# Performance work log

Hardware: AMD Instinct MI355X
Metric: run time of the kernel (lower is better)

## Reference

```python
import jax, jax.numpy as jnp
import numpy as np

B, C, W, H, N = 8, 128, 48, 48, 8192


def setup_inputs() -> dict:
    key = jax.random.key(0)
    ks = jax.random.split(key, 16)
    s = 1.0 / np.sqrt(C)
    inp = {
        "feat0": jax.random.normal(ks[0], (B, C, W, H), jnp.float32),
        "feat1": jax.random.normal(ks[1], (B, C, N), jnp.float32),
        "geo_embed": jax.random.normal(ks[2], (B, W * H, C), jnp.float32),
        # Linear weights stored as [in, out]; biases [out].
        "Wq": jax.random.normal(ks[3], (C, C), jnp.float32) * s,
        "bq": jnp.zeros((C,), jnp.float32),
        "Wk": jax.random.normal(ks[4], (C, C), jnp.float32) * s,
        "bk": jnp.zeros((C,), jnp.float32),
        "Wv": jax.random.normal(ks[5], (C, C), jnp.float32) * s,
        "bv": jnp.zeros((C,), jnp.float32),
        "Wo": jax.random.normal(ks[6], (C, C), jnp.float32) * s,
        "bo": jnp.zeros((C,), jnp.float32),
        "Wg": jax.random.normal(ks[7], (C, C), jnp.float32) * s,
        "bg": jnp.zeros((C,), jnp.float32),
        "Wgate": jax.random.normal(ks[8], (2 * C, 1), jnp.float32) * (1.0 / np.sqrt(2 * C)),
        "bgate": jnp.zeros((1,), jnp.float32),
    }
    return inp


def reference(feat0, feat1, geo_embed, Wq, bq, Wk, bk, Wv, bv, Wo, bo, Wg, bg, Wgate, bgate):
    b, c, w, h = feat0.shape
    # b c w h -> b (w h) c
    q_in = feat0.reshape(b, c, w * h).transpose(0, 2, 1)
    pq = q_in @ Wq + bq  # [b, wh, c]

    geo = geo_embed @ Wg + bg  # [b, wh, c]
    gate = jax.nn.sigmoid(jnp.concatenate([pq, geo], axis=-1) @ Wgate + bgate)  # [b, wh, 1]
    pq = pq + gate * geo

    kv_in = feat1.transpose(0, 2, 1)  # [b, n, c]
    pk = kv_in @ Wk + bk
    pv = kv_in @ Wv + bv

    energy = jnp.einsum('bqc,bnc->bqn', pq, pk)  # [b, wh, n]
    # NOTE: original scales AFTER softmax (non-standard, faithful):
    attention = jax.nn.softmax(energy, axis=-1) / jnp.sqrt(jnp.asarray(c, energy.dtype))
    out = jnp.einsum('bqn,bnc->bqc', attention, pv) @ Wo + bo  # [b, wh, c]
    out = out.transpose(0, 2, 1).reshape(b, c, w, h)

    geo_r = geo.transpose(0, 2, 1).reshape(b, c, w, h)
    out = out * (1.0 + jax.nn.sigmoid(geo_r))
    out = out + feat0
    return out
```

## Files before the change

kernel.cpp:

```cpp
#include <hip/hip_runtime.h>

#define B_ 8
#define C_ 128
#define WH_ 2304
#define N_ 8192

typedef unsigned short u16;
typedef float f32x4 __attribute__((ext_vector_type(4)));
typedef short s16x8 __attribute__((ext_vector_type(8)));
typedef short s16x4 __attribute__((ext_vector_type(4)));
typedef unsigned int u32x2 __attribute__((ext_vector_type(2)));

typedef const unsigned int __attribute__((address_space(1))) ga_u32;
typedef unsigned int __attribute__((address_space(3))) lds_u32;

#define LOG2E 1.4426950408889634f
#define MOFF  64.0f

__device__ __forceinline__ float bf2f(u16 u){
    union { unsigned int i; float f; } x; x.i = ((unsigned int)u) << 16; return x.f;
}
__device__ __forceinline__ u16 f2bf(float f){
    union { float f; unsigned int i; } x; x.f = f;
    unsigned int r = x.i + 0x7fffu + ((x.i >> 16) & 1u);
    return (u16)(r >> 16);
}
__device__ __forceinline__ unsigned int cvtpk(float a, float b){
    unsigned int r;
    asm("v_cvt_pk_bf16_f32 %0, %1, %2" : "=v"(r) : "v"(a), "v"(b));
    return r;
}
__device__ __forceinline__ int swz(int row, int col){
    return row*128 + ((((col >> 3) ^ (row & 15)) << 3) | (col & 7));
}
__device__ __forceinline__ f32x4 fzero(){ f32x4 z = {0.f, 0.f, 0.f, 0.f}; return z; }
__device__ __forceinline__ f32x4 fmoff(){ f32x4 z = {-MOFF, -MOFF, -MOFF, -MOFF}; return z; }
__device__ __forceinline__ f32x4 mfma16(s16x8 a, s16x8 b, f32x4 c){
    return __builtin_amdgcn_mfma_f32_16x16x32_bf16(a, b, c, 0, 0, 0);
}
__device__ __forceinline__ void gld16(const void* g, void* l){
    __builtin_amdgcn_global_load_lds((ga_u32*)g, (lds_u32*)l, 16, 0, 0);
}
__device__ __forceinline__ s16x8 ldsf(const u16* p){ return *(const s16x8*)p; }
__device__ __forceinline__ s16x8 cvt8(const float* p){
    s16x8 r;
    #pragma unroll
    for (int j = 0; j < 8; j++) r[j] = (short)f2bf(p[j]);
    return r;
}

__global__ __launch_bounds__(256) void k_prep(
    const float* __restrict__ Wq, const float* __restrict__ Wk,
    const float* __restrict__ Wv, const float* __restrict__ Wo,
    const float* __restrict__ Wg, u16* __restrict__ Wt)
{
    const int gid = blockIdx.x*256 + threadIdx.x;
    const int mi = gid >> 14, e = gid & 16383;
    const int o = e >> 7, i = e & 127;
    const float* src = (mi==0)?Wq:(mi==1)?Wk:(mi==2)?Wv:(mi==3)?Wo:Wg;
    Wt[mi*16384 + o*128 + i] = f2bf(src[i*128 + o]);
}

__device__ __forceinline__ void proj_kv_body(
    u16* SB, int blk,
    const float* __restrict__ feat1,
    const float* __restrict__ bk, const float* __restrict__ bv,
    const u16* __restrict__ Wt,
    u16* __restrict__ Kb, u16* __restrict__ Vb)
{
    const int t = threadIdx.x;
    const int b = blk >> 7;
    const int n0 = (blk & 127) * 64;
    const int lane = t & 63, w = t >> 6, qq = lane >> 4, m = lane & 15;
    const int nr = n0 + w*16 + m;
    s16x8 aA[4];
    #pragma unroll
    for (int kt = 0; kt < 4; kt++){
        #pragma unroll
        for (int j = 0; j < 8; j++)
            aA[kt][j] = (short)f2bf(feat1[((size_t)b*C_ + kt*32 + qq*8 + j)*N_ + nr]);
    }
    const u16* WkT = Wt + 16384;
    const u16* WvT = Wt + 32768;
    f32x4 acc[8];
    #pragma unroll
    for (int ct = 0; ct < 8; ct++) acc[ct] = fzero();
    #pragma unroll
    for (int kt = 0; kt < 4; kt++){
        #pragma unroll
        for (int ct = 0; ct < 8; ct++){
            const s16x8 bf = *(const s16x8*)&WkT[(ct*16 + m)*128 + kt*32 + qq*8];
            acc[ct] = mfma16(aA[kt], bf, acc[ct]);
        }
    }
    #pragma unroll
    for (int ct = 0; ct < 8; ct++){
        const int col = ct*16 + m;
        const float bkv = bk[col];
        #pragma unroll
        for (int i = 0; i < 4; i++)
            SB[swz(w*16 + qq*4 + i, col)] = f2bf(acc[ct][i] + bkv);
    }
    #pragma unroll
    for (int j = 0; j < 4; j++){
        const int chunk = j*64 + lane;
        const int row = w*16 + (chunk >> 4);
        const int cb = chunk & 15;
        s16x8 v = ldsf(&SB[row*128 + ((cb ^ (row & 15)) << 3)]);
        *(s16x8*)&Kb[((size_t)b*N_ + n0 + row)*C_ + cb*8] = v;
    }
    #pragma unroll
    for (int ct = 0; ct < 8; ct++) acc[ct] = fzero();
    #pragma unroll
    for (int kt = 0; kt < 4; kt++){
        #pragma unroll
        for (int ct = 0; ct < 8; ct++){
            const s16x8 bf = *(const s16x8*)&WvT[(ct*16 + m)*128 + kt*32 + qq*8];
            acc[ct] = mfma16(aA[kt], bf, acc[ct]);
        }
    }
    #pragma unroll
    for (int ct = 0; ct < 8; ct++){
        const int col = ct*16 + m;
        const float bvv = bv[col];
        u32x2 pk;
        pk.x = cvtpk(acc[ct][0] + bvv, acc[ct][1] + bvv);
        pk.y = cvtpk(acc[ct][2] + bvv, acc[ct][3] + bvv);
        *(u32x2*)&Vb[((size_t)b*C_ + col)*N_ + n0 + w*16 + qq*4] = pk;
    }
}

__device__ __forceinline__ void proj_qg_body(
    u16* SB, int blk,
    const float* __restrict__ feat0, const float* __restrict__ geo,
    const float* __restrict__ bq, const float* __restrict__ bg,
    const float* __restrict__ Wgate, const float* __restrict__ bgate,
    const u16* __restrict__ Wt,
    u16* __restrict__ Qb, u16* __restrict__ Gb)
{
    const int t = threadIdx.x;
    const int b = blk / 36;
    const int r0 = (blk % 36) * 64;
    const int lane = t & 63, w = t >> 6, qq = lane >> 4, m = lane & 15;
    const int ar = w*16 + m;
    s16x8 aQ[4], aG[4];
    #pragma unroll
    for (int kt = 0; kt < 4; kt++){
        #pragma unroll
        for (int j = 0; j < 8; j++)
            aQ[kt][j] = (short)f2bf(feat0[((size_t)b*C_ + kt*32 + qq*8 + j)*WH_ + r0 + ar]);
        aG[kt] = cvt8(&geo[((size_t)b*WH_ + r0 + ar)*C_ + kt*32 + qq*8]);
    }
    f32x4 accq[8], accg[8];
    #pragma unroll
    for (int ct = 0; ct < 8; ct++){ accq[ct] = fzero(); accg[ct] = fzero(); }
    #pragma unroll
    for (int kt = 0; kt < 4; kt++){
        #pragma unroll
        for (int ct = 0; ct < 8; ct++){
            const int bn = ct*16 + m;
            const s16x8 b1 = *(const s16x8*)&Wt[bn*128 + kt*32 + qq*8];
            const s16x8 b2 = *(const s16x8*)&Wt[65536 + bn*128 + kt*32 + qq*8];
            accq[ct] = mfma16(aQ[kt], b1, accq[ct]);
            accg[ct] = mfma16(aG[kt], b2, accg[ct]);
        }
    }
    #pragma unroll
    for (int ct = 0; ct < 8; ct++){
        const int col = ct*16 + m;
        const float bqv = bq[col], bgv = bg[col];
        #pragma unroll
        for (int i = 0; i < 4; i++){ accq[ct][i] += bqv; accg[ct][i] += bgv; }
    }
    float w1v[8], w2v[8];
    #pragma unroll
    for (int ct = 0; ct < 8; ct++){
        const int col = ct*16 + m;
        w1v[ct] = Wgate[col]; w2v[ct] = Wgate[C_ + col];
    }
    const float bg0 = bgate[0];
    float gate[4];
    #pragma unroll
    for (int i = 0; i < 4; i++){
        float p = 0.f;
        #pragma unroll
        for (int ct = 0; ct < 8; ct++)
            p += accq[ct][i] * w1v[ct] + accg[ct][i] * w2v[ct];
        #pragma unroll
        for (int off = 1; off < 16; off <<= 1) p += __shfl_xor(p, off, 64);
        gate[i] = 1.f / (1.f + __expf(-(p + bg0)));
    }
    #pragma unroll
    for (int ct = 0; ct < 8; ct++){
        #pragma unroll
        for (int i = 0; i < 4; i++){
            const float pq = accq[ct][i] + gate[i] * accg[ct][i];
            SB[swz(w*16 + qq*4 + i, ct*16 + m)] = f2bf(pq * LOG2E);
        }
    }
    #pragma unroll
    for (int j = 0; j < 4; j++){
        const int chunk = j*64 + lane;
        const int row = w*16 + (chunk >> 4);
        const int cb = chunk & 15;
        s16x8 v = ldsf(&SB[row*128 + ((cb ^ (row & 15)) << 3)]);
        *(s16x8*)&Qb[((size_t)b*WH_ + r0 + row)*C_ + cb*8] = v;
    }
    #pragma unroll
    for (int ct = 0; ct < 8; ct++){
        #pragma unroll
        for (int i = 0; i < 4; i++)
            SB[swz(w*16 + qq*4 + i, ct*16 + m)] = f2bf(accg[ct][i]);
    }
    #pragma unroll
    for (int j = 0; j < 4; j++){
        const int chunk = j*64 + lane;
        const int row = w*16 + (chunk >> 4);
        const int cb = chunk & 15;
        s16x8 v = ldsf(&SB[row*128 + ((cb ^ (row & 15)) << 3)]);
        *(s16x8*)&Gb[((size_t)b*WH_ + r0 + row)*C_ + cb*8] = v;
    }
}

__global__ __launch_bounds__(256, 3) void k_proj(
    const float* __restrict__ feat1,
    const float* __restrict__ bk, const float* __restrict__ bv,
    const float* __restrict__ feat0, const float* __restrict__ geo,
    const float* __restrict__ bq, const float* __restrict__ bg,
    const float* __restrict__ Wgate, const float* __restrict__ bgate,
    const u16* __restrict__ Wt,
    u16* __restrict__ Kb, u16* __restrict__ Vb,
    u16* __restrict__ Qb, u16* __restrict__ Gb)
{
    __shared__ __attribute__((aligned(16))) u16 SB[64*128];
    if (blockIdx.x < 1024)
        proj_kv_body(SB, blockIdx.x, feat1, bk, bv, Wt, Kb, Vb);
    else
        proj_qg_body(SB, blockIdx.x - 1024, feat0, geo, bq, bg, Wgate, bgate, Wt, Qb, Gb);
}

__global__ __launch_bounds__(1024, 4) void k_flash(
    const u16* __restrict__ Qb, const u16* __restrict__ Kb, const u16* __restrict__ Vb,
    u16* __restrict__ Opart, float* __restrict__ Lp)
{
    __shared__ __attribute__((aligned(16))) u16 KP0[128*128];
    __shared__ __attribute__((aligned(16))) u16 KP1[128*128];
    __shared__ __attribute__((aligned(16))) u16 Vt0[128*128];
    __shared__ __attribute__((aligned(16))) u16 Vt1[128*128];
    const int t = threadIdx.x;
    const int lane = t & 63, w = t >> 6;
    const int q = lane >> 4, m = lane & 15;
    const int b = blockIdx.x & 7;
    const int s = blockIdx.x >> 3;

    f32x4 o[8];
    f32x4 l_acc;
    s16x8 qf[4];
    s16x8 ones8;
    #pragma unroll
    for (int j = 0; j < 8; j++) ones8[j] = (short)0x3F80;

    auto issue = [&](int k){
        const int u = s*18 + k;
        const int n0 = (u & 63) * 128;
        u16* KPd = (k & 1) ? KP1 : KP0;
        u16* Vtd = (k & 1) ? Vt1 : Vt0;
        #pragma unroll
        for (int j = 0; j < 2; j++){
            const int r = w*8 + j*4 + q;
            const int pr = (r & 96) | ((r & 12) << 1) | ((r & 16) >> 2) | (r & 3);
            gld16(Kb + ((size_t)b*N_ + n0 + pr)*C_ + ((m ^ (r & 15)) << 3), &KPd[(w*8 + j*4)*128]);
            gld16(Vb + ((size_t)b*C_ + r)*N_ + n0 + ((m ^ (r & 15)) << 3), &Vtd[(w*8 + j*4)*128]);
        }
    };
    auto load_q = [&](int qb){
        const size_t qrow0 = (size_t)b*WH_ + qb*256;
        #pragma unroll
        for (int kt = 0; kt < 4; kt++)
            qf[kt] = *(const s16x8*)&Qb[(qrow0 + w*16 + m)*C_ + kt*32 + q*8];
    };
    auto zero_acc = [&](){
        #pragma unroll
        for (int ct = 0; ct < 8; ct++) o[ct] = fzero();
        l_acc = fzero();
    };
    auto flush = [&](int qb){
        const int sf = (qb * 64) / 18;
        const size_t pbase = ((size_t)(b*9 + qb)*5 + (s - sf)) * 256;
        #pragma unroll
        for (int ct = 0; ct < 8; ct++){
            u32x2 pk;
            pk.x = cvtpk(o[ct][0], o[ct][1]);
            pk.y = cvtpk(o[ct][2], o[ct][3]);
            *(u32x2*)&Opart[(pbase + w*16 + m)*128 + ct*16 + q*4] = pk;
        }
        if (q == 0) Lp[pbase + w*16 + m] = l_acc[0];
    };

    issue(0);
    int cur_qb = (s*18) >> 6;
    load_q(cur_qb);
    zero_acc();

    for (int k = 0; k < 18; k++){
        __syncthreads();
        if (k < 17) issue(k + 1);
        const u16* KPc = (k & 1) ? KP1 : KP0;
        const u16* Vtc = (k & 1) ? Vt1 : Vt0;

        #pragma unroll
        for (int h = 0; h < 2; h++){
            s16x4 pexp[4];
            #pragma unroll
            for (int n2 = 0; n2 < 4; n2++){
                const int nt = h*4 + n2;
                f32x4 s0 = fmoff();
                const int bn = nt*16 + m;
                #pragma unroll
                for (int kt = 0; kt < 4; kt++){
                    s16x8 kf = ldsf(&KPc[bn*128 + (((kt*4 + q) ^ (bn & 15)) << 3)]);
                    s0 = mfma16(kf, qf[kt], s0);
                }
                union { u32x2 u; s16x4 v; } pp;
                pp.u.x = cvtpk(exp2f(s0[0]), exp2f(s0[1]));
                pp.u.y = cvtpk(exp2f(s0[2]), exp2f(s0[3]));
                pexp[n2] = pp.v;
            }
            const s16x8 p80 = __builtin_shufflevector(pexp[0], pexp[1], 0,1,2,3,4,5,6,7);
            const s16x8 p81 = __builtin_shufflevector(pexp[2], pexp[3], 0,1,2,3,4,5,6,7);
            l_acc = mfma16(ones8, p80, l_acc);
            l_acc = mfma16(ones8, p81, l_acc);
            #pragma unroll
            for (int ct = 0; ct < 8; ct++){
                const int cc = ct*16 + m;
                const int pair0 = h*2;
                s16x8 vf0 = ldsf(&Vtc[cc*128 + ((((pair0+0)*4 + q) ^ (cc & 15)) << 3)]);
                s16x8 vf1 = ldsf(&Vtc[cc*128 + ((((pair0+1)*4 + q) ^ (cc & 15)) << 3)]);
                o[ct] = mfma16(vf0, p80, o[ct]);
                o[ct] = mfma16(vf1, p81, o[ct]);
            }
        }
        const int nqb = (k < 17) ? ((s*18 + k + 1) >> 6) : -1;
        if (nqb != cur_qb){
            flush(cur_qb);
            if (nqb >= 0){ load_q(nqb); zero_acc(); cur_qb = nqb; }
        }
    }
}

__global__ __launch_bounds__(256, 4) void k_out(
    const u16* __restrict__ Opart, const float* __restrict__ Lp,
    const float* __restrict__ bo, const u16* __restrict__ Wt,
    const u16* __restrict__ Gb, const float* __restrict__ feat0,
    float* __restrict__ outp)
{
    __shared__ __attribute__((aligned(16))) u16 AO[64*128];
    const int t = threadIdx.x;
    const int r36 = blockIdx.x % 36;
    const int b = blockIdx.x / 36;
    const int qb = r36 >> 2, quarter = r36 & 3;
    const int gr0 = qb*256 + quarter*64;
    const int qt2 = b*9 + qb;
    const u16* WoT = Wt + 49152;
    const float rsC = 0.088388347648318447f;
    const int sf = (qb*64) / 18;
    const int sl = (qb*64 + 63) / 18;
    const int cnt = sl - sf + 1;
    for (int idx = t; idx < 64*16; idx += 256){
        int r = idx >> 4, cb = idx & 15;
        float num[8];
        #pragma unroll
        for (int j = 0; j < 8; j++) num[j] = 0.f;
        float den = 0.f;
        for (int ss = 0; ss < cnt; ss++){
            const size_t base = ((size_t)qt2*5 + ss)*256 + quarter*64 + r;
            s16x8 v = *(const s16x8*)&Opart[base*128 + cb*8];
            #pragma unroll
            for (int j = 0; j < 8; j++) num[j] += bf2f((u16)v[j]);
            den += Lp[base];
        }
        const float sc = rsC / den;
        s16x8 o8;
        #pragma unroll
        for (int j = 0; j < 8; j++) o8[j] = (short)f2bf(num[j] * sc);
        *(s16x8*)&AO[r*128 + ((cb ^ (r & 15)) << 3)] = o8;
    }
    __syncthreads();
    const int lane = t & 63, w = t >> 6;
    const int q = lane >> 4, m = lane & 15;
    f32x4 acc[8];
    #pragma unroll
    for (int ct = 0; ct < 8; ct++) acc[ct] = fzero();
    #pragma unroll
    for (int kt = 0; kt < 4; kt++){
        const int ar = w*16 + m;
        const s16x8 a0 = ldsf(&AO[ar*128 + (((kt*4 + q) ^ (ar & 15)) << 3)]);
        #pragma unroll
        for (int ct = 0; ct < 8; ct++){
            const s16x8 bb = *(const s16x8*)&WoT[(ct*16 + m)*128 + kt*32 + q*8];
            acc[ct] = mfma16(a0, bb, acc[ct]);
        }
    }
    u16* Tr = AO;
    #pragma unroll
    for (int ct = 0; ct < 8; ct++){
        const int col = ct*16 + m;
        const float bov = bo[col];
        #pragma unroll
        for (int i = 0; i < 4; i++){
            const int rl = w*16 + q*4 + i;
            const float gv = bf2f(Gb[((size_t)b*WH_ + gr0 + rl)*C_ + col]);
            const float sg = 1.f / (1.f + __expf(-gv));
            Tr[swz(rl, col)] = f2bf((acc[ct][i] + bov) * (1.f + sg));
        }
    }
    __syncthreads();
    for (int idx = t; idx < 64*128; idx += 256){
        int c = idx >> 6, wh = idx & 63;
        float v = bf2f(Tr[swz(wh, c)]) + feat0[(size_t)(b*C_ + c)*WH_ + gr0 + wh];
        outp[(size_t)(b*C_ + c)*WH_ + gr0 + wh] = v;
    }
}

extern "C" void kernel_launch(void* const* d_in, const int* in_sizes, int n_in,
                              void* d_out, int out_size, void* d_ws, size_t ws_size,
                              hipStream_t stream)
{
    (void)in_sizes; (void)n_in; (void)out_size; (void)ws_size;
    const float* feat0 = (const float*)d_in[0];
    const float* feat1 = (const float*)d_in[1];
    const float* geo   = (const float*)d_in[2];
    const float* Wq = (const float*)d_in[3];  const float* bq = (const float*)d_in[4];
    const float* Wk = (const float*)d_in[5];  const float* bk = (const float*)d_in[6];
    const float* Wv = (const float*)d_in[7];  const float* bv = (const float*)d_in[8];
    const float* Wo = (const float*)d_in[9];  const float* bo = (const float*)d_in[10];
    const float* Wg = (const float*)d_in[11]; const float* bg = (const float*)d_in[12];
    const float* Wgate = (const float*)d_in[13]; const float* bgate = (const float*)d_in[14];
    float* outp = (float*)d_out;
    char* ws = (char*)d_ws;
    size_t off = 0;
    auto alloc = [&](size_t bytes) -> void* {
        void* p = (void*)(ws + off);
        off += (bytes + 255) & ~(size_t)255;
        return p;
    };
    u16* Qb = (u16*)alloc((size_t)B_*WH_*C_*2);
    u16* Gb = (u16*)alloc((size_t)B_*WH_*C_*2);
    u16* Kb = (u16*)alloc((size_t)B_*N_*C_*2);
    u16* Vb = (u16*)alloc((size_t)B_*N_*C_*2);
    u16* Opart = (u16*)alloc((size_t)72*5*256*128*2);
    float* Lp  = (float*)alloc((size_t)72*5*256*4);
    u16* Wt = (u16*)alloc((size_t)5*16384*2);

    k_prep <<<dim3(320),  dim3(256),  0, stream>>>(Wq, Wk, Wv, Wo, Wg, Wt);
    k_proj <<<dim3(1312), dim3(256),  0, stream>>>(feat1, bk, bv, feat0, geo, bq, bg,
                                                   Wgate, bgate, Wt, Kb, Vb, Qb, Gb);
    k_flash<<<dim3(256),  dim3(1024), 0, stream>>>(Qb, Kb, Vb, Opart, Lp);
    k_out  <<<dim3(288),  dim3(256),  0, stream>>>(Opart, Lp, bo, Wt, Gb, feat0, outp);
}
```

Before: 272.4 us.

## Have each flash wave process two 16-row query tiles to reuse K/V fragments

Halves the flash-attention block to 512 threads and makes every wave handle 32 query rows (two 16-row tiles) instead of 16. Each K and V fragment read from LDS now feeds two MFMA chains, halving LDS read traffic per MFMA, and the cooperative global-to-LDS load loop grows to cover the same 128-row tiles with fewer threads. The cost is doubled accumulator and Q-fragment registers per thread and fewer waves per block to hide latency.

```diff
diff --git a/kernel.cpp b/kernel.cpp
--- a/kernel.cpp
+++ b/kernel.cpp
@@ -239,7 +239,7 @@
         proj_qg_body(SB, blockIdx.x - 1024, feat0, geo, bq, bg, Wgate, bgate, Wt, Qb, Gb);
 }
 
-__global__ __launch_bounds__(1024, 4) void k_flash(
+__global__ __launch_bounds__(512, 2) void k_flash(
     const u16* __restrict__ Qb, const u16* __restrict__ Kb, const u16* __restrict__ Vb,
     u16* __restrict__ Opart, float* __restrict__ Lp)
 {
@@ -250,12 +250,13 @@
     const int t = threadIdx.x;
     const int lane = t & 63, w = t >> 6;
     const int q = lane >> 4, m = lane & 15;
+    const int rw = w * 32;
     const int b = blockIdx.x & 7;
     const int s = blockIdx.x >> 3;
 
-    f32x4 o[8];
-    f32x4 l_acc;
-    s16x8 qf[4];
+    f32x4 o[2][8];
+    f32x4 l_acc[2];
+    s16x8 qf[2][4];
     s16x8 ones8;
     #pragma unroll
     for (int j = 0; j < 8; j++) ones8[j] = (short)0x3F80;
@@ -266,35 +267,44 @@
         u16* KPd = (k & 1) ? KP1 : KP0;
         u16* Vtd = (k & 1) ? Vt1 : Vt0;
         #pragma unroll
-        for (int j = 0; j < 2; j++){
-            const int r = w*8 + j*4 + q;
+        for (int j = 0; j < 4; j++){
+            const int r = w*16 + j*4 + q;
             const int pr = (r & 96) | ((r & 12) << 1) | ((r & 16) >> 2) | (r & 3);
-            gld16(Kb + ((size_t)b*N_ + n0 + pr)*C_ + ((m ^ (r & 15)) << 3), &KPd[(w*8 + j*4)*128]);
-            gld16(Vb + ((size_t)b*C_ + r)*N_ + n0 + ((m ^ (r & 15)) << 3), &Vtd[(w*8 + j*4)*128]);
+            gld16(Kb + ((size_t)b*N_ + n0 + pr)*C_ + ((m ^ (r & 15)) << 3), &KPd[(w*16 + j*4)*128]);
+            gld16(Vb + ((size_t)b*C_ + r)*N_ + n0 + ((m ^ (r & 15)) << 3), &Vtd[(w*16 + j*4)*128]);
         }
     };
     auto load_q = [&](int qb){
         const size_t qrow0 = (size_t)b*WH_ + qb*256;
         #pragma unroll
-        for (int kt = 0; kt < 4; kt++)
-            qf[kt] = *(const s16x8*)&Qb[(qrow0 + w*16 + m)*C_ + kt*32 + q*8];
+        for (int rt = 0; rt < 2; rt++){
+            #pragma unroll
+            for (int kt = 0; kt < 4; kt++)
+                qf[rt][kt] = *(const s16x8*)&Qb[(qrow0 + rw + rt*16 + m)*C_ + kt*32 + q*8];
+        }
     };
     auto zero_acc = [&](){
         #pragma unroll
-        for (int ct = 0; ct < 8; ct++) o[ct] = fzero();
-        l_acc = fzero();
+        for (int ct = 0; ct < 8; ct++){ o[0][ct] = fzero(); o[1][ct] = fzero(); }
+        l_acc[0] = fzero(); l_acc[1] = fzero();
     };
     auto flush = [&](int qb){
         const int sf = (qb * 64) / 18;
         const size_t pbase = ((size_t)(b*9 + qb)*5 + (s - sf)) * 256;
         #pragma unroll
         for (int ct = 0; ct < 8; ct++){
-            u32x2 pk;
-            pk.x = cvtpk(o[ct][0], o[ct][1]);
-            pk.y = cvtpk(o[ct][2], o[ct][3]);
-            *(u32x2*)&Opart[(pbase + w*16 + m)*128 + ct*16 + q*4] = pk;
-        }
-        if (q == 0) Lp[pbase + w*16 + m] = l_acc[0];
+            #pragma unroll
+            for (int rt = 0; rt < 2; rt++){
+                u32x2 pk;
+                pk.x = cvtpk(o[rt][ct][0], o[rt][ct][1]);
+                pk.y = cvtpk(o[rt][ct][2], o[rt][ct][3]);
+                *(u32x2*)&Opart[(pbase + rw + rt*16 + m)*128 + ct*16 + q*4] = pk;
+            }
+        }
+        if (q == 0){
+            Lp[pbase + rw + m] = l_acc[0][0];
+            Lp[pbase + rw + 16 + m] = l_acc[1][0];
+        }
     };
 
     issue(0);
@@ -310,34 +320,43 @@
 
         #pragma unroll
         for (int h = 0; h < 2; h++){
-            s16x4 pexp[4];
+            s16x4 pexp[4][2];
             #pragma unroll
             for (int n2 = 0; n2 < 4; n2++){
                 const int nt = h*4 + n2;
-                f32x4 s0 = fmoff();
+                f32x4 s0 = fmoff(), s1 = fmoff();
                 const int bn = nt*16 + m;
                 #pragma unroll
                 for (int kt = 0; kt < 4; kt++){
                     s16x8 kf = ldsf(&KPc[bn*128 + (((kt*4 + q) ^ (bn & 15)) << 3)]);
-                    s0 = mfma16(kf, qf[kt], s0);
+                    s0 = mfma16(kf, qf[0][kt], s0);
+                    s1 = mfma16(kf, qf[1][kt], s1);
                 }
-                union { u32x2 u; s16x4 v; } pp;
-                pp.u.x = cvtpk(exp2f(s0[0]), exp2f(s0[1]));
-                pp.u.y = cvtpk(exp2f(s0[2]), exp2f(s0[3]));
-                pexp[n2] = pp.v;
+                union { u32x2 u; s16x4 v; } p0, p1;
+                p0.u.x = cvtpk(exp2f(s0[0]), exp2f(s0[1]));
+                p0.u.y = cvtpk(exp2f(s0[2]), exp2f(s0[3]));
+                p1.u.x = cvtpk(exp2f(s1[0]), exp2f(s1[1]));
+                p1.u.y = cvtpk(exp2f(s1[2]), exp2f(s1[3]));
+                pexp[n2][0] = p0.v; pexp[n2][1] = p1.v;
             }
-            const s16x8 p80 = __builtin_shufflevector(pexp[0], pexp[1], 0,1,2,3,4,5,6,7);
-            const s16x8 p81 = __builtin_shufflevector(pexp[2], pexp[3], 0,1,2,3,4,5,6,7);
-            l_acc = mfma16(ones8, p80, l_acc);
-            l_acc = mfma16(ones8, p81, l_acc);
+            const s16x8 pA0 = __builtin_shufflevector(pexp[0][0], pexp[1][0], 0,1,2,3,4,5,6,7);
+            const s16x8 pB0 = __builtin_shufflevector(pexp[2][0], pexp[3][0], 0,1,2,3,4,5,6,7);
+            const s16x8 pA1 = __builtin_shufflevector(pexp[0][1], pexp[1][1], 0,1,2,3,4,5,6,7);
+            const s16x8 pB1 = __builtin_shufflevector(pexp[2][1], pexp[3][1], 0,1,2,3,4,5,6,7);
+            l_acc[0] = mfma16(ones8, pA0, l_acc[0]);
+            l_acc[0] = mfma16(ones8, pB0, l_acc[0]);
+            l_acc[1] = mfma16(ones8, pA1, l_acc[1]);
+            l_acc[1] = mfma16(ones8, pB1, l_acc[1]);
             #pragma unroll
             for (int ct = 0; ct < 8; ct++){
                 const int cc = ct*16 + m;
                 const int pair0 = h*2;
                 s16x8 vf0 = ldsf(&Vtc[cc*128 + ((((pair0+0)*4 + q) ^ (cc & 15)) << 3)]);
                 s16x8 vf1 = ldsf(&Vtc[cc*128 + ((((pair0+1)*4 + q) ^ (cc & 15)) << 3)]);
-                o[ct] = mfma16(vf0, p80, o[ct]);
-                o[ct] = mfma16(vf1, p81, o[ct]);
+                o[0][ct] = mfma16(vf0, pA0, o[0][ct]);
+                o[0][ct] = mfma16(vf1, pB0, o[0][ct]);
+                o[1][ct] = mfma16(vf0, pA1, o[1][ct]);
+                o[1][ct] = mfma16(vf1, pB1, o[1][ct]);
             }
         }
         const int nqb = (k < 17) ? ((s*18 + k + 1) >> 6) : -1;
@@ -452,9 +471,9 @@
     float* Lp  = (float*)alloc((size_t)72*5*256*4);
     u16* Wt = (u16*)alloc((size_t)5*16384*2);
 
-    k_prep <<<dim3(320),  dim3(256),  0, stream>>>(Wq, Wk, Wv, Wo, Wg, Wt);
-    k_proj <<<dim3(1312), dim3(256),  0, stream>>>(feat1, bk, bv, feat0, geo, bq, bg,
-                                                   Wgate, bgate, Wt, Kb, Vb, Qb, Gb);
-    k_flash<<<dim3(256),  dim3(1024), 0, stream>>>(Qb, Kb, Vb, Opart, Lp);
-    k_out  <<<dim3(288),  dim3(256),  0, stream>>>(Opart, Lp, bo, Wt, Gb, feat0, outp);
-}
+    k_prep <<<dim3(320),  dim3(256), 0, stream>>>(Wq, Wk, Wv, Wo, Wg, Wt);
+    k_proj <<<dim3(1312), dim3(256), 0, stream>>>(feat1, bk, bv, feat0, geo, bq, bg,
+                                                  Wgate, bgate, Wt, Kb, Vb, Qb, Gb);
+    k_flash<<<dim3(256),  dim3(512), 0, stream>>>(Qb, Kb, Vb, Opart, Lp);
+    k_out  <<<dim3(288),  dim3(256), 0, stream>>>(Opart, Lp, bo, Wt, Gb, feat0, outp);
+}
```

After: 272.0 us. Within noise of the previous version (-0.1%).
